# Kernel tuning notes

Measured on AMD Instinct MI355X. Metric: run time of the kernel, lower is better.

## Reference

```python
import jax, jax.numpy as jnp
import numpy as np

BS, E, A, TE, TA = 128, 32, 8, 8, 4
V, WD, HD = 30522, 300, 1024


def gru_last(x, lengths, Wih, Whh, bih, bhh):
    """Single-layer unidirectional GRU (torch gate math); returns h at step lengths-1.
    x: [N, T, D], lengths: [N] (>=1)."""
    N, T, D = x.shape
    xp = jnp.einsum('ntd,gd->ntg', x, Wih) + bih  # [N, T, 3D]
    h0 = jnp.zeros((N, D), x.dtype)

    def step(h, args):
        xpt, t = args
        gh = h @ Whh.T + bhh
        xr, xz, xn = jnp.split(xpt, 3, axis=-1)
        hr, hz, hn = jnp.split(gh, 3, axis=-1)
        r = jax.nn.sigmoid(xr + hr)
        z = jax.nn.sigmoid(xz + hz)
        n = jnp.tanh(xn + r * hn)
        h_new = (1.0 - z) * n + z * h
        h = jnp.where((t < lengths)[:, None], h_new, h)  # freeze after length
        return h, None

    hT, _ = jax.lax.scan(step, h0, (jnp.transpose(xp, (1, 0, 2)), jnp.arange(T)))
    return hT


def setup_inputs() -> dict:
    key = jax.random.key(0)
    ks = jax.random.split(key, 20)
    s = 0.05
    p = lambda k, shp: jax.random.normal(k, shp, dtype=jnp.float32) * s
    return {
        'entity_tokens': jax.random.randint(ks[0], (BS, E, TE), 0, V),
        'entity_lengths': jax.random.randint(ks[1], (BS, E), 1, TE + 1),
        'entity_padding_mask': jnp.zeros((BS, E, TE), dtype=bool),
        'entity_attribute_tokens': jax.random.randint(ks[2], (BS, E, A, TA), 0, V),
        'entity_attribute_lengths': jax.random.randint(ks[3], (BS, E, A), 1, TA + 1),
        'entity_attribute_padding_mask': jnp.zeros((BS, E, A, TA), dtype=bool),
        'emb_table': p(ks[4], (V, WD)),
        'Wih_ent': p(ks[5], (3 * WD, WD)),
        'Whh_ent': p(ks[6], (3 * WD, WD)),
        'bih_ent': jnp.zeros((3 * WD,), jnp.float32),
        'bhh_ent': jnp.zeros((3 * WD,), jnp.float32),
        'Wih_attr': p(ks[7], (3 * WD, WD)),
        'Whh_attr': p(ks[8], (3 * WD, WD)),
        'bih_attr': jnp.zeros((3 * WD,), jnp.float32),
        'bhh_attr': jnp.zeros((3 * WD,), jnp.float32),
        'Wfc': p(ks[9], (HD, WD)),
        'bfc': jnp.zeros((HD,), jnp.float32),
        'Wg': p(ks[10], (HD, HD)),
        'a_src': p(ks[11], (HD,)),
        'a_dst': p(ks[12], (HD,)),
    }


def reference(entity_tokens, entity_lengths, entity_padding_mask,
              entity_attribute_tokens, entity_attribute_lengths, entity_attribute_padding_mask,
              emb_table, Wih_ent, Whh_ent, bih_ent, bhh_ent,
              Wih_attr, Whh_attr, bih_attr, bhh_attr,
              Wfc, bfc, Wg, a_src, a_dst):
    bs, nE, tE = entity_tokens.shape
    nA, tA = entity_attribute_tokens.shape[2], entity_attribute_tokens.shape[3]
    G = bs * nE
    N = nA + 1  # 1 entity node + nA attribute nodes per small star graph

    # --- embed entity phrases (GRU over tokens, take last valid state) ---
    ent_len = jnp.clip(entity_lengths.reshape(-1), 1, None)
    ent_x = emb_table[entity_tokens.reshape(G, tE)]  # [G, tE, WD]
    ent_h = gru_last(ent_x, ent_len, Wih_ent, Whh_ent, bih_ent, bhh_ent)
    ent = jax.nn.relu(ent_h @ Wfc.T + bfc)  # [G, HD]

    # --- embed attribute phrases ---
    at_len = jnp.clip(entity_attribute_lengths.reshape(-1), 1, None)
    at_x = emb_table[entity_attribute_tokens.reshape(G * nA, tA)]
    at_h = gru_last(at_x, at_len, Wih_attr, Whh_attr, bih_attr, bhh_attr)
    attr = jax.nn.relu(at_h @ Wfc.T + bfc).reshape(G, nA, -1)  # [G, nA, HD]

    # --- adjacency: entity node 0 linked to each valid attribute; self loop on node 0 ---
    valid = ((~entity_attribute_padding_mask).sum(-1) > 0).reshape(G, nA).astype(jnp.float32)
    adj = jnp.zeros((G, N, N), jnp.float32)
    adj = adj.at[:, 1:, 0].set(valid)
    adj = adj.at[:, 0, 0].set(1.0)
    adj = adj + jnp.transpose(adj, (0, 2, 1))
    adj = adj > 1e-5  # bool mask

    # --- GAT-style masked node attention ---
    nodes = jnp.concatenate([ent[:, None, :], attr], axis=1)  # [G, N, HD]
    h = nodes @ Wg.T
    es = h @ a_src  # [G, N]
    ed = h @ a_dst
    e = jax.nn.leaky_relu(es[:, :, None] + ed[:, None, :], 0.2)
    e = jnp.where(adj, e, -1e9)
    alpha = jax.nn.softmax(e, axis=-1)
    out = jax.nn.elu(jnp.einsum('gij,gjd->gid', alpha, h))

    entity_embeds = out[:, 0, :].reshape(bs, nE, -1)  # hidden_dim == embed_dim -> no fc_out
    return entity_embeds
```

## Files before the change

### kernel.cpp

```cpp
#include <hip/hip_runtime.h>
#include <math.h>

namespace {

typedef unsigned short bf16_t;
typedef __bf16  bf16x8_t __attribute__((ext_vector_type(8)));
typedef float   f32x4_t  __attribute__((ext_vector_type(4)));
typedef unsigned int u32x4 __attribute__((ext_vector_type(4)));

constexpr int G     = 4096;
constexpr int GA    = 32768;
constexpr int WDIM  = 300;
constexpr int KPAD  = 320;
constexpr int HDIM  = 1024;
constexpr int NNODE = 9;
constexpr int MROWS = G * NNODE;
constexpr int TE_   = 8;
constexpr int TA_   = 4;
constexpr int V_    = 30522;
constexpr int VP    = 30592;
constexpr int PROJW = 1024;

__device__ __forceinline__ float bf2f(bf16_t b) {
    union { unsigned int u; float f; } v; v.u = ((unsigned int)b) << 16; return v.f;
}
__device__ __forceinline__ bf16_t f2bf(float f) {
    union { float f; unsigned int u; } v; v.f = f;
    unsigned int r = v.u + 0x7FFFu + ((v.u >> 16) & 1u);
    return (bf16_t)(r >> 16);
}

template<int MODE>
__global__ __launch_bounds__(256)
void mfma_gemm(const bf16_t* __restrict__ A, const bf16_t* __restrict__ B,
               void* __restrict__ Cv, int lda, int ldb, int ldc, int K)
{
    __shared__ bf16_t As[128 * 32];
    __shared__ bf16_t Bs[128 * 32];

    const int tid  = threadIdx.x;
    const int w    = tid >> 6;
    const int lane = tid & 63;
    const int wr = w >> 1, wc = w & 1;
    const int lr = lane & 15;
    const int lk = lane >> 4;
    const int m0 = blockIdx.x * 128, n0 = blockIdx.y * 128;

    const int r0 = tid >> 2;
    const int cc = (tid & 3) * 8;
    const bf16_t* Arow0 = A + (size_t)(m0 + r0) * lda + cc;
    const bf16_t* Arow1 = Arow0 + (size_t)64 * lda;
    const bf16_t* Brow0 = B + (size_t)(n0 + r0) * ldb + cc;
    const bf16_t* Brow1 = Brow0 + (size_t)64 * ldb;

    f32x4_t acc[4][4];
#pragma unroll
    for (int i = 0; i < 4; ++i)
#pragma unroll
        for (int j = 0; j < 4; ++j) acc[i][j] = {0.f, 0.f, 0.f, 0.f};

    for (int k0 = 0; k0 < K; k0 += 32) {
        const uint4 a0 = *(const uint4*)(Arow0 + k0);
        const uint4 a1 = *(const uint4*)(Arow1 + k0);
        const uint4 b0 = *(const uint4*)(Brow0 + k0);
        const uint4 b1 = *(const uint4*)(Brow1 + k0);
        __syncthreads();
        *(uint4*)&As[r0 * 32 + cc]        = a0;
        *(uint4*)&As[(r0 + 64) * 32 + cc] = a1;
        *(uint4*)&Bs[r0 * 32 + cc]        = b0;
        *(uint4*)&Bs[(r0 + 64) * 32 + cc] = b1;
        __syncthreads();

        bf16x8_t af[4], bfr[4];
#pragma unroll
        for (int i = 0; i < 4; ++i) {
            af[i]  = *(const bf16x8_t*)&As[(wr * 64 + i * 16 + lr) * 32 + lk * 8];
            bfr[i] = *(const bf16x8_t*)&Bs[(wc * 64 + i * 16 + lr) * 32 + lk * 8];
        }
#pragma unroll
        for (int mi = 0; mi < 4; ++mi)
#pragma unroll
            for (int ni = 0; ni < 4; ++ni)
                acc[mi][ni] = __builtin_amdgcn_mfma_f32_16x16x32_bf16(
                    af[mi], bfr[ni], acc[mi][ni], 0, 0, 0);
    }

#pragma unroll
    for (int mi = 0; mi < 4; ++mi) {
#pragma unroll
        for (int ni = 0; ni < 4; ++ni) {
            const int n = n0 + wc * 64 + ni * 16 + lr;
#pragma unroll
            for (int r = 0; r < 4; ++r) {
                const int m = m0 + wr * 64 + mi * 16 + lk * 4 + r;
                const float v = acc[mi][ni][r];
                if (MODE == 0)
                    ((bf16_t*)Cv)[(size_t)m * ldc + n] = f2bf(v);
                else
                    ((float*)Cv)[(size_t)m * ldc + n] = v > 0.f ? v : expm1f(v);
            }
        }
    }
}

__global__ __launch_bounds__(512)
void gru_step_fused(const bf16_t* __restrict__ hin,
                    bf16_t* __restrict__ hout,
                    const bf16_t* __restrict__ Whh3i,
                    const bf16_t* __restrict__ proj,
                    const int* __restrict__ tokens,
                    const int* __restrict__ lengths,
                    const float* __restrict__ bih, const float* __restrict__ bhh,
                    int T, int t)
{
    constexpr int GSTRF = 123;
    __shared__ __align__(16) bf16_t As[128 * 32];
    __shared__ __align__(16) bf16_t Bs[128 * 32];
    __shared__ float gsm[128 * GSTRF];

    const int tid = threadIdx.x;
    const int w = tid >> 6, lane = tid & 63;
    const int lr = lane & 15, lk = lane >> 4;
    const int wr = w >> 2, wc = w & 3;
    const int m0 = blockIdx.x * 128;
    const int nb = blockIdx.y;
    const int n0 = nb * 120;

    const int sr = tid >> 2, sc = (tid & 3) * 8;
    const bf16_t* Ap = hin   + (size_t)(m0 + sr) * KPAD + sc;
    const bf16_t* Bp = Whh3i + (size_t)(n0 + sr) * KPAD + sc;

    f32x4_t acc[4][2];
#pragma unroll
    for (int mi = 0; mi < 4; ++mi)
#pragma unroll
        for (int ni = 0; ni < 2; ++ni) acc[mi][ni] = {0.f, 0.f, 0.f, 0.f};

    for (int k0 = 0; k0 < KPAD; k0 += 32) {
        const uint4 av = *(const uint4*)(Ap + k0);
        const uint4 bv = *(const uint4*)(Bp + k0);
        __syncthreads();
        *(uint4*)&As[sr * 32 + sc] = av;
        *(uint4*)&Bs[sr * 32 + sc] = bv;
        __syncthreads();

        bf16x8_t af[4], bfr[2];
#pragma unroll
        for (int mi = 0; mi < 4; ++mi)
            af[mi] = *(const bf16x8_t*)&As[(wr * 64 + mi * 16 + lr) * 32 + lk * 8];
#pragma unroll
        for (int ni = 0; ni < 2; ++ni)
            bfr[ni] = *(const bf16x8_t*)&Bs[(wc * 32 + ni * 16 + lr) * 32 + lk * 8];
#pragma unroll
        for (int mi = 0; mi < 4; ++mi)
#pragma unroll
            for (int ni = 0; ni < 2; ++ni)
                acc[mi][ni] = __builtin_amdgcn_mfma_f32_16x16x32_bf16(
                    af[mi], bfr[ni], acc[mi][ni], 0, 0, 0);
    }

#pragma unroll
    for (int ni = 0; ni < 2; ++ni) {
        const int col = wc * 32 + ni * 16 + lr;
        if (col < 120) {
#pragma unroll
            for (int mi = 0; mi < 4; ++mi)
#pragma unroll
                for (int r = 0; r < 4; ++r)
                    gsm[(wr * 64 + mi * 16 + lk * 4 + r) * GSTRF + col]
                        = acc[mi][ni][r];
        }
    }
    __syncthreads();

    const int ml = tid >> 2, q = tid & 3;
    if (nb == 7 && q >= 2) return;
    const int m  = m0 + ml;
    const int jb = nb * 40 + q * 10;
    int len = lengths[m]; if (len < 1) len = 1;
    const bool act = (t < len);
    const int tok = tokens[(size_t)m * T + t];

    const unsigned int* xpp =
        (const unsigned int*)(proj + (size_t)tok * PROJW + n0 + q * 30);
    unsigned int xw[15];
#pragma unroll
    for (int i = 0; i < 15; ++i) xw[i] = xpp[i];

    const unsigned int* hop = (const unsigned int*)(hin + (size_t)m * KPAD + jb);
    unsigned int hw[5];
#pragma unroll
    for (int i = 0; i < 5; ++i) hw[i] = hop[i];

    unsigned int ow[5];
#pragma unroll
    for (int u = 0; u < 10; ++u) {
        const int j = jb + u;
        const bf16_t hob = (bf16_t)((u & 1) ? (hw[u >> 1] >> 16) : (hw[u >> 1] & 0xffff));
        const float hold = bf2f(hob);
        float hv = hold;
        if (act) {
            const int e0 = 3 * u;
            const float xr = bf2f((bf16_t)((e0 & 1)       ? (xw[e0 >> 1] >> 16)       : (xw[e0 >> 1] & 0xffff)));
            const float xz = bf2f((bf16_t)(((e0 + 1) & 1) ? (xw[(e0 + 1) >> 1] >> 16) : (xw[(e0 + 1) >> 1] & 0xffff)));
            const float xn = bf2f((bf16_t)(((e0 + 2) & 1) ? (xw[(e0 + 2) >> 1] >> 16) : (xw[(e0 + 2) >> 1] & 0xffff)));
            const int nl = q * 30 + 3 * u;
            const float g0 = gsm[ml * GSTRF + nl];
            const float g1 = gsm[ml * GSTRF + nl + 1];
            const float g2 = gsm[ml * GSTRF + nl + 2];
            const float rr = 1.f / (1.f + expf(-(g0 + xr + bih[j] + bhh[j])));
            const float zz = 1.f / (1.f + expf(-(g1 + xz + bih[WDIM + j] + bhh[WDIM + j])));
            const float nn = tanhf(xn + bih[2 * WDIM + j] + rr * (g2 + bhh[2 * WDIM + j]));
            hv = (1.f - zz) * nn + zz * hold;
        }
        const bf16_t hb_ = f2bf(hv);
        if ((u & 1) == 0) ow[u >> 1] = hb_;
        else              ow[u >> 1] |= ((unsigned int)hb_) << 16;
    }
    unsigned int* outp = (unsigned int*)(hout + (size_t)m * KPAD + jb);
#pragma unroll
    for (int i = 0; i < 5; ++i) outp[i] = ow[i];
}

__global__ __launch_bounds__(256)
void fc_nodes_esed(const bf16_t* __restrict__ hEnt, const bf16_t* __restrict__ hAtt,
                   const bf16_t* __restrict__ WfcB, const float* __restrict__ bfc,
                   const float* __restrict__ asW, const float* __restrict__ adW,
                   bf16_t* __restrict__ nodes, float* __restrict__ es, float* __restrict__ ed)
{
    constexpr int ASTR = 328;
    __shared__ bf16_t As[64 * ASTR];
    __shared__ bf16_t Bs[64 * 32];
    __shared__ const bf16_t* rowp[64];

    const int tid = threadIdx.x;
    const int w = tid >> 6, lane = tid & 63;
    const int lr = lane & 15, lk = lane >> 4;
    const int m0 = blockIdx.x * 64;

    if (tid < 64) {
        const int m = m0 + tid;
        const int g = m / NNODE, i = m - g * NNODE;
        rowp[tid] = (i == 0) ? (hEnt + (size_t)g * KPAD)
                             : (hAtt + (size_t)(g * 8 + (i - 1)) * KPAD);
    }
    __syncthreads();

#pragma unroll
    for (int it = 0; it < 10; ++it) {
        const int i = tid + 256 * it;
        const int row = i / 40, c8 = (i - row * 40) * 8;
        const uint4 v = *(const uint4*)(rowp[row] + c8);
        *(uint4*)&As[row * ASTR + c8] = v;
    }
    __syncthreads();

    float esa[4] = {0.f, 0.f, 0.f, 0.f};
    float eda[4] = {0.f, 0.f, 0.f, 0.f};

    for (int nt = 0; nt < 16; ++nt) {
        const int n0 = nt * 64;
        f32x4_t acc[4];
#pragma unroll
        for (int ni = 0; ni < 4; ++ni) acc[ni] = {0.f, 0.f, 0.f, 0.f};

        for (int k0 = 0; k0 < KPAD; k0 += 32) {
            const int rr_ = tid >> 2, c8 = (tid & 3) * 8;
            const uint4 bv = *(const uint4*)(WfcB + (size_t)(n0 + rr_) * KPAD + k0 + c8);
            __syncthreads();
            *(uint4*)&Bs[rr_ * 32 + c8] = bv;
            __syncthreads();

            const bf16x8_t af = *(const bf16x8_t*)&As[(w * 16 + lr) * ASTR + k0 + lk * 8];
#pragma unroll
            for (int ni = 0; ni < 4; ++ni) {
                const bf16x8_t bfr = *(const bf16x8_t*)&Bs[(ni * 16 + lr) * 32 + lk * 8];
                acc[ni] = __builtin_amdgcn_mfma_f32_16x16x32_bf16(af, bfr, acc[ni], 0, 0, 0);
            }
        }

#pragma unroll
        for (int ni = 0; ni < 4; ++ni) {
            const int n = n0 + ni * 16 + lr;
            const float aw = asW[n], dw = adW[n], bb = bfc[n];
#pragma unroll
            for (int r = 0; r < 4; ++r) {
                float v = acc[ni][r] + bb;
                v = v > 0.f ? v : 0.f;
                const int m = m0 + w * 16 + lk * 4 + r;
                nodes[(size_t)m * HDIM + n] = f2bf(v);
                esa[r] = fmaf(v, aw, esa[r]);
                eda[r] = fmaf(v, dw, eda[r]);
            }
        }
    }

#pragma unroll
    for (int r = 0; r < 4; ++r) {
        float s = esa[r], d = eda[r];
#pragma unroll
        for (int mask = 1; mask < 16; mask <<= 1) {
            s += __shfl_xor(s, mask, 64);
            d += __shfl_xor(d, mask, 64);
        }
        if (lr == 0) {
            const int m = m0 + w * 16 + lk * 4 + r;
            es[m] = s; ed[m] = d;
        }
    }
}

__global__ __launch_bounds__(256)
void convert_emb_kernel(const float* __restrict__ emb, bf16_t* __restrict__ embB)
{
    const int idx = blockIdx.x * 256 + threadIdx.x;
    if (idx >= V_ * 40) return;
    const int row = idx / 40, c8 = (idx - row * 40) * 8;
    bf16_t o[8];
#pragma unroll
    for (int e = 0; e < 8; ++e) {
        const int c = c8 + e;
        o[e] = (c < WDIM) ? f2bf(emb[(size_t)row * WDIM + c]) : (bf16_t)0;
    }
    *(ushort4*)(embB + (size_t)row * KPAD + c8)     = *(ushort4*)&o[0];
    *(ushort4*)(embB + (size_t)row * KPAD + c8 + 4) = *(ushort4*)&o[4];
}

__global__ __launch_bounds__(256)
void build_w3i_kernel(const float* __restrict__ W, bf16_t* __restrict__ dst)
{
    const int idx = blockIdx.x * 256 + threadIdx.x;
    if (idx >= HDIM * KPAD) return;
    const int n = idx / KPAD, k = idx - n * KPAD;
    float v = 0.f;
    if (n < 960) {
        const int j = n / 3, g = n - j * 3;
        if (j < WDIM && k < WDIM)
            v = W[(size_t)(g * WDIM + j) * WDIM + k];
    }
    dst[idx] = f2bf(v);
}

__global__ __launch_bounds__(256)
void build_wfc_kernel(const float* __restrict__ Wfc, bf16_t* __restrict__ Wb)
{
    const int idx = blockIdx.x * 256 + threadIdx.x;
    if (idx >= HDIM * KPAD) return;
    const int n = idx / KPAD, k = idx - n * KPAD;
    Wb[idx] = f2bf(k < WDIM ? Wfc[(size_t)n * WDIM + k] : 0.f);
}

__global__ __launch_bounds__(256)
void build_wg_kernel(const float* __restrict__ Wg, bf16_t* __restrict__ Wb)
{
    const int idx = blockIdx.x * 256 + threadIdx.x;
    Wb[idx] = f2bf(Wg[idx]);
}

__global__ __launch_bounds__(256)
void asw_kernel(const float* __restrict__ Wg,
                const float* __restrict__ a_src, const float* __restrict__ a_dst,
                float* __restrict__ asW, float* __restrict__ adW)
{
    const int k = blockIdx.x * 256 + threadIdx.x;
    float s = 0.f, d = 0.f;
    for (int n = 0; n < HDIM; ++n) {
        const float w = Wg[(size_t)n * HDIM + k];
        s = fmaf(a_src[n], w, s);
        d = fmaf(a_dst[n], w, d);
    }
    asW[k] = s; adW[k] = d;
}

__global__ __launch_bounds__(256)
void attn_mix_kernel(const bf16_t* __restrict__ nodes,
                     const float* __restrict__ es, const float* __restrict__ ed,
                     bf16_t* __restrict__ mixed)
{
    const int g = blockIdx.x;
    const float e0 = es[(size_t)g * NNODE];
    const float* edg = ed + (size_t)g * NNODE;

    float w[NNODE], mx = -1e30f;
#pragma unroll
    for (int j = 0; j < NNODE; ++j) {
        float v = e0 + edg[j];
        v = v >= 0.f ? v : 0.2f * v;
        w[j] = v; mx = fmaxf(mx, v);
    }
    float denom = 0.f;
#pragma unroll
    for (int j = 0; j < NNODE; ++j) { w[j] = expf(w[j] - mx); denom += w[j]; }
    const float inv = 1.f / denom;

    const int c = threadIdx.x * 4;
    float4 acc = {0.f, 0.f, 0.f, 0.f};
#pragma unroll
    for (int j = 0; j < NNODE; ++j) {
        const float a = w[j] * inv;
        const ushort4 h4 = *(const ushort4*)(nodes + (size_t)(g * NNODE + j) * HDIM + c);
        acc.x = fmaf(a, bf2f(h4.x), acc.x);
        acc.y = fmaf(a, bf2f(h4.y), acc.y);
        acc.z = fmaf(a, bf2f(h4.z), acc.z);
        acc.w = fmaf(a, bf2f(h4.w), acc.w);
    }
    ushort4 o;
    o.x = f2bf(acc.x); o.y = f2bf(acc.y); o.z = f2bf(acc.z); o.w = f2bf(acc.w);
    *(ushort4*)(mixed + (size_t)g * HDIM + c) = o;
}

constexpr size_t SZ_EMBB  = (size_t)VP * KPAD * sizeof(bf16_t);
constexpr size_t SZ_PROJ  = (size_t)VP * PROJW * sizeof(bf16_t);
constexpr size_t SZ_HATT  = (size_t)GA * KPAD * sizeof(bf16_t);
constexpr size_t SZ_HENT  = (size_t)G * KPAD * sizeof(bf16_t);
constexpr size_t SZ_WIH3  = (size_t)HDIM * KPAD * sizeof(bf16_t);
constexpr size_t SZ_WHH3E = (size_t)HDIM * KPAD * sizeof(bf16_t);
constexpr size_t SZ_WFC   = (size_t)HDIM * KPAD * sizeof(bf16_t);
constexpr size_t SZ_WG    = (size_t)HDIM * HDIM * sizeof(bf16_t);
constexpr size_t SZ_AW    = (size_t)HDIM * sizeof(float);
constexpr size_t SZ_VEC   = (size_t)MROWS * sizeof(float);
constexpr size_t SZ_NODE  = (size_t)MROWS * HDIM * sizeof(bf16_t);
constexpr size_t SZ_MIX   = (size_t)G * HDIM * sizeof(bf16_t);
constexpr size_t WS_NEED  = SZ_EMBB + SZ_PROJ + 2 * SZ_HATT + 2 * SZ_HENT +
                            SZ_WIH3 + 2 * SZ_WHH3E + SZ_WFC + SZ_WG +
                            2 * SZ_AW + 2 * SZ_VEC;
static_assert(SZ_NODE <= SZ_EMBB + SZ_PROJ, "nodes overlays embB+proj");
static_assert(SZ_MIX  <= 2 * SZ_HATT,       "mixed overlays hAtt pair");

}

extern "C" void kernel_launch(void* const* d_in, const int* in_sizes, int n_in,
                              void* d_out, int out_size, void* d_ws, size_t ws_size,
                              hipStream_t stream)
{
    (void)in_sizes; (void)n_in; (void)out_size;
    if (ws_size < WS_NEED) return;

    const int*   ent_tok  = (const int*)  d_in[0];
    const int*   ent_len  = (const int*)  d_in[1];
    const int*   at_tok   = (const int*)  d_in[3];
    const int*   at_len   = (const int*)  d_in[4];
    const float* emb      = (const float*)d_in[6];
    const float* Wih_ent  = (const float*)d_in[7];
    const float* Whh_ent  = (const float*)d_in[8];
    const float* bih_ent  = (const float*)d_in[9];
    const float* bhh_ent  = (const float*)d_in[10];
    const float* Wih_attr = (const float*)d_in[11];
    const float* Whh_attr = (const float*)d_in[12];
    const float* bih_attr = (const float*)d_in[13];
    const float* bhh_attr = (const float*)d_in[14];
    const float* Wfc      = (const float*)d_in[15];
    const float* bfc      = (const float*)d_in[16];
    const float* Wg       = (const float*)d_in[17];
    const float* a_src    = (const float*)d_in[18];
    const float* a_dst    = (const float*)d_in[19];
    float* out = (float*)d_out;

    char* p = (char*)d_ws;
    bf16_t* embB  = (bf16_t*)p; p += SZ_EMBB;
    bf16_t* proj  = (bf16_t*)p; p += SZ_PROJ;
    bf16_t* hAtt[2];
    hAtt[0] = (bf16_t*)p; p += SZ_HATT;
    hAtt[1] = (bf16_t*)p; p += SZ_HATT;
    bf16_t* hEnt   = (bf16_t*)p; p += SZ_HENT;
    bf16_t* hEnt2  = (bf16_t*)p; p += SZ_HENT;
    bf16_t* Wih3   = (bf16_t*)p; p += SZ_WIH3;
    bf16_t* Whh3_a = (bf16_t*)p; p += SZ_WHH3E;
    bf16_t* Whh3_e = (bf16_t*)p; p += SZ_WHH3E;
    bf16_t* WfcB   = (bf16_t*)p; p += SZ_WFC;
    bf16_t* WgB    = (bf16_t*)p; p += SZ_WG;
    float*  asW    = (float*)p;  p += SZ_AW;
    float*  adW    = (float*)p;  p += SZ_AW;
    float*  es     = (float*)p;  p += SZ_VEC;
    float*  ed     = (float*)p;  p += SZ_VEC;
    bf16_t* nodes  = embB;
    bf16_t* mixed  = hAtt[0];

    hipMemsetAsync(hAtt[0], 0, SZ_HATT, stream);
    hipMemsetAsync(hAtt[1], 0, SZ_HATT, stream);
    hipMemsetAsync(hEnt,  0, SZ_HENT, stream);
    hipMemsetAsync(hEnt2, 0, SZ_HENT, stream);

    convert_emb_kernel<<<dim3((V_ * 40 + 255) / 256), 256, 0, stream>>>(emb, embB);
    build_w3i_kernel<<<dim3(HDIM * KPAD / 256), 256, 0, stream>>>(Wih_attr, Wih3);
    build_w3i_kernel<<<dim3(HDIM * KPAD / 256), 256, 0, stream>>>(Whh_attr, Whh3_a);
    build_w3i_kernel<<<dim3(HDIM * KPAD / 256), 256, 0, stream>>>(Whh_ent, Whh3_e);
    build_wfc_kernel<<<dim3(HDIM * KPAD / 256), 256, 0, stream>>>(Wfc, WfcB);
    build_wg_kernel<<<dim3(HDIM * HDIM / 256), 256, 0, stream>>>(Wg, WgB);
    asw_kernel<<<dim3(HDIM / 256), 256, 0, stream>>>(Wg, a_src, a_dst, asW, adW);

    mfma_gemm<0><<<dim3(VP / 128, PROJW / 128), 256, 0, stream>>>(
        embB, Wih3, proj, KPAD, KPAD, PROJW, KPAD);

    for (int t = 0; t < TA_; ++t)
        gru_step_fused<<<dim3(GA / 128, 8), 512, 0, stream>>>(
            hAtt[t & 1], hAtt[(t + 1) & 1], Whh3_a, proj, at_tok, at_len,
            bih_attr, bhh_attr, TA_, t);

    build_w3i_kernel<<<dim3(HDIM * KPAD / 256), 256, 0, stream>>>(Wih_ent, Wih3);
    mfma_gemm<0><<<dim3(VP / 128, PROJW / 128), 256, 0, stream>>>(
        embB, Wih3, proj, KPAD, KPAD, PROJW, KPAD);

    bf16_t* hb[2] = { hEnt, hEnt2 };
    for (int t = 0; t < TE_; ++t)
        gru_step_fused<<<dim3(G / 128, 8), 512, 0, stream>>>(
            hb[t & 1], hb[(t + 1) & 1], Whh3_e, proj, ent_tok, ent_len,
            bih_ent, bhh_ent, TE_, t);

    fc_nodes_esed<<<dim3(MROWS / 64), 256, 0, stream>>>(
        hEnt, hAtt[0], WfcB, bfc, asW, adW, nodes, es, ed);

    attn_mix_kernel<<<dim3(G), 256, 0, stream>>>(nodes, es, ed, mixed);

    mfma_gemm<2><<<dim3(G / 128, HDIM / 128), 256, 0, stream>>>(
        mixed, WgB, out, HDIM, HDIM, HDIM, HDIM);
}
```

Baseline: 779.6 us.

## Pad GEMM LDS rows and split fc_nodes into tiled GEMM plus es/ed kernel

The shared-memory tiles in the generic MFMA GEMM get a row stride of 40 instead of 32, which is meant to reduce LDS bank conflicts on fragment reads. The fused fc_nodes_esed kernel, which gave each block 64 rows and looped over all 1024 output columns, is replaced by a 2D-tiled 128x128 GEMM. Its es/ed attention-score dot products move into a separate kernel that re-reads the bf16 nodes. This adds parallelism and reuse to the FC GEMM, at the cost of an extra launch and an extra pass over the nodes buffer. es/ed are now computed from bf16-rounded values rather than fp32, a small numerical change.

```diff
diff --git a/kernel.cpp b/kernel.cpp
--- a/kernel.cpp
+++ b/kernel.cpp
@@ -35,8 +35,9 @@
 void mfma_gemm(const bf16_t* __restrict__ A, const bf16_t* __restrict__ B,
                void* __restrict__ Cv, int lda, int ldb, int ldc, int K)
 {
-    __shared__ bf16_t As[128 * 32];
-    __shared__ bf16_t Bs[128 * 32];
+    constexpr int AST = 40;
+    __shared__ __align__(16) bf16_t As[128 * AST];
+    __shared__ __align__(16) bf16_t Bs[128 * AST];
 
     const int tid  = threadIdx.x;
     const int w    = tid >> 6;
@@ -65,17 +66,17 @@
         const uint4 b0 = *(const uint4*)(Brow0 + k0);
         const uint4 b1 = *(const uint4*)(Brow1 + k0);
         __syncthreads();
-        *(uint4*)&As[r0 * 32 + cc]        = a0;
-        *(uint4*)&As[(r0 + 64) * 32 + cc] = a1;
-        *(uint4*)&Bs[r0 * 32 + cc]        = b0;
-        *(uint4*)&Bs[(r0 + 64) * 32 + cc] = b1;
+        *(uint4*)&As[r0 * AST + cc]        = a0;
+        *(uint4*)&As[(r0 + 64) * AST + cc] = a1;
+        *(uint4*)&Bs[r0 * AST + cc]        = b0;
+        *(uint4*)&Bs[(r0 + 64) * AST + cc] = b1;
         __syncthreads();
 
         bf16x8_t af[4], bfr[4];
 #pragma unroll
         for (int i = 0; i < 4; ++i) {
-            af[i]  = *(const bf16x8_t*)&As[(wr * 64 + i * 16 + lr) * 32 + lk * 8];
-            bfr[i] = *(const bf16x8_t*)&Bs[(wc * 64 + i * 16 + lr) * 32 + lk * 8];
+            af[i]  = *(const bf16x8_t*)&As[(wr * 64 + i * 16 + lr) * AST + lk * 8];
+            bfr[i] = *(const bf16x8_t*)&Bs[(wc * 64 + i * 16 + lr) * AST + lk * 8];
         }
 #pragma unroll
         for (int mi = 0; mi < 4; ++mi)
@@ -223,22 +224,24 @@
 }
 
 __global__ __launch_bounds__(256)
-void fc_nodes_esed(const bf16_t* __restrict__ hEnt, const bf16_t* __restrict__ hAtt,
+void fc_nodes_gemm(const bf16_t* __restrict__ hEnt, const bf16_t* __restrict__ hAtt,
                    const bf16_t* __restrict__ WfcB, const float* __restrict__ bfc,
-                   const float* __restrict__ asW, const float* __restrict__ adW,
-                   bf16_t* __restrict__ nodes, float* __restrict__ es, float* __restrict__ ed)
-{
-    constexpr int ASTR = 328;
-    __shared__ bf16_t As[64 * ASTR];
-    __shared__ bf16_t Bs[64 * 32];
-    __shared__ const bf16_t* rowp[64];
-
-    const int tid = threadIdx.x;
-    const int w = tid >> 6, lane = tid & 63;
-    const int lr = lane & 15, lk = lane >> 4;
-    const int m0 = blockIdx.x * 64;
-
-    if (tid < 64) {
+                   bf16_t* __restrict__ nodes)
+{
+    constexpr int AST = 40;
+    __shared__ __align__(16) bf16_t As[128 * AST];
+    __shared__ __align__(16) bf16_t Bs[128 * AST];
+    __shared__ const bf16_t* rowp[128];
+
+    const int tid  = threadIdx.x;
+    const int w    = tid >> 6;
+    const int lane = tid & 63;
+    const int wr = w >> 1, wc = w & 1;
+    const int lr = lane & 15;
+    const int lk = lane >> 4;
+    const int m0 = blockIdx.x * 128, n0 = blockIdx.y * 128;
+
+    if (tid < 128) {
         const int m = m0 + tid;
         const int g = m / NNODE, i = m - g * NNODE;
         rowp[tid] = (i == 0) ? (hEnt + (size_t)g * KPAD)
@@ -246,68 +249,96 @@
     }
     __syncthreads();
 
-#pragma unroll
-    for (int it = 0; it < 10; ++it) {
-        const int i = tid + 256 * it;
-        const int row = i / 40, c8 = (i - row * 40) * 8;
-        const uint4 v = *(const uint4*)(rowp[row] + c8);
-        *(uint4*)&As[row * ASTR + c8] = v;
-    }
-    __syncthreads();
-
-    float esa[4] = {0.f, 0.f, 0.f, 0.f};
-    float eda[4] = {0.f, 0.f, 0.f, 0.f};
-
-    for (int nt = 0; nt < 16; ++nt) {
-        const int n0 = nt * 64;
-        f32x4_t acc[4];
-#pragma unroll
-        for (int ni = 0; ni < 4; ++ni) acc[ni] = {0.f, 0.f, 0.f, 0.f};
-
-        for (int k0 = 0; k0 < KPAD; k0 += 32) {
-            const int rr_ = tid >> 2, c8 = (tid & 3) * 8;
-            const uint4 bv = *(const uint4*)(WfcB + (size_t)(n0 + rr_) * KPAD + k0 + c8);
-            __syncthreads();
-            *(uint4*)&Bs[rr_ * 32 + c8] = bv;
-            __syncthreads();
-
-            const bf16x8_t af = *(const bf16x8_t*)&As[(w * 16 + lr) * ASTR + k0 + lk * 8];
-#pragma unroll
-            for (int ni = 0; ni < 4; ++ni) {
-                const bf16x8_t bfr = *(const bf16x8_t*)&Bs[(ni * 16 + lr) * 32 + lk * 8];
-                acc[ni] = __builtin_amdgcn_mfma_f32_16x16x32_bf16(af, bfr, acc[ni], 0, 0, 0);
+    const int r0 = tid >> 2;
+    const int cc = (tid & 3) * 8;
+    const bf16_t* Arow0 = rowp[r0] + cc;
+    const bf16_t* Arow1 = rowp[r0 + 64] + cc;
+    const bf16_t* Brow0 = WfcB + (size_t)(n0 + r0) * KPAD + cc;
+    const bf16_t* Brow1 = Brow0 + (size_t)64 * KPAD;
+
+    f32x4_t acc[4][4];
+#pragma unroll
+    for (int i = 0; i < 4; ++i)
+#pragma unroll
+        for (int j = 0; j < 4; ++j) acc[i][j] = {0.f, 0.f, 0.f, 0.f};
+
+    for (int k0 = 0; k0 < KPAD; k0 += 32) {
+        const uint4 a0 = *(const uint4*)(Arow0 + k0);
+        const uint4 a1 = *(const uint4*)(Arow1 + k0);
+        const uint4 b0 = *(const uint4*)(Brow0 + k0);
+        const uint4 b1 = *(const uint4*)(Brow1 + k0);
+        __syncthreads();
+        *(uint4*)&As[r0 * AST + cc]        = a0;
+        *(uint4*)&As[(r0 + 64) * AST + cc] = a1;
+        *(uint4*)&Bs[r0 * AST + cc]        = b0;
+        *(uint4*)&Bs[(r0 + 64) * AST + cc] = b1;
+        __syncthreads();
+
+        bf16x8_t af[4], bfr[4];
+#pragma unroll
+        for (int i = 0; i < 4; ++i) {
+            af[i]  = *(const bf16x8_t*)&As[(wr * 64 + i * 16 + lr) * AST + lk * 8];
+            bfr[i] = *(const bf16x8_t*)&Bs[(wc * 64 + i * 16 + lr) * AST + lk * 8];
+        }
+#pragma unroll
+        for (int mi = 0; mi < 4; ++mi)
+#pragma unroll
+            for (int ni = 0; ni < 4; ++ni)
+                acc[mi][ni] = __builtin_amdgcn_mfma_f32_16x16x32_bf16(
+                    af[mi], bfr[ni], acc[mi][ni], 0, 0, 0);
+    }
+
+#pragma unroll
+    for (int mi = 0; mi < 4; ++mi) {
+#pragma unroll
+        for (int ni = 0; ni < 4; ++ni) {
+            const int n = n0 + wc * 64 + ni * 16 + lr;
+            const float bb = bfc[n];
+#pragma unroll
+            for (int r = 0; r < 4; ++r) {
+                const int m = m0 + wr * 64 + mi * 16 + lk * 4 + r;
+                float v = acc[mi][ni][r] + bb;
+                v = v > 0.f ? v : 0.f;
+                nodes[(size_t)m * HDIM + n] = f2bf(v);
             }
         }
-
-#pragma unroll
-        for (int ni = 0; ni < 4; ++ni) {
-            const int n = n0 + ni * 16 + lr;
-            const float aw = asW[n], dw = adW[n], bb = bfc[n];
-#pragma unroll
-            for (int r = 0; r < 4; ++r) {
-                float v = acc[ni][r] + bb;
-                v = v > 0.f ? v : 0.f;
-                const int m = m0 + w * 16 + lk * 4 + r;
-                nodes[(size_t)m * HDIM + n] = f2bf(v);
-                esa[r] = fmaf(v, aw, esa[r]);
-                eda[r] = fmaf(v, dw, eda[r]);
-            }
-        }
-    }
-
-#pragma unroll
-    for (int r = 0; r < 4; ++r) {
-        float s = esa[r], d = eda[r];
-#pragma unroll
-        for (int mask = 1; mask < 16; mask <<= 1) {
-            s += __shfl_xor(s, mask, 64);
-            d += __shfl_xor(d, mask, 64);
-        }
-        if (lr == 0) {
-            const int m = m0 + w * 16 + lk * 4 + r;
-            es[m] = s; ed[m] = d;
-        }
-    }
+    }
+}
+
+__global__ __launch_bounds__(256)
+void esed_kernel(const bf16_t* __restrict__ nodes,
+                 const float* __restrict__ asW, const float* __restrict__ adW,
+                 float* __restrict__ es, float* __restrict__ ed)
+{
+    const int m    = (blockIdx.x * 256 + threadIdx.x) >> 6;
+    const int lane = threadIdx.x & 63;
+    const bf16_t* row = nodes + (size_t)m * HDIM;
+
+    const uint4 v0 = *(const uint4*)(row + lane * 8);
+    const uint4 v1 = *(const uint4*)(row + 512 + lane * 8);
+
+    float s = 0.f, d = 0.f;
+    const unsigned int* w0 = (const unsigned int*)&v0;
+    const unsigned int* w1 = (const unsigned int*)&v1;
+#pragma unroll
+    for (int e = 0; e < 4; ++e) {
+        const int c0 = lane * 8 + 2 * e;
+        const float x0 = bf2f((bf16_t)(w0[e] & 0xffff));
+        const float x1 = bf2f((bf16_t)(w0[e] >> 16));
+        s = fmaf(x0, asW[c0], s);     s = fmaf(x1, asW[c0 + 1], s);
+        d = fmaf(x0, adW[c0], d);     d = fmaf(x1, adW[c0 + 1], d);
+        const int c1 = 512 + lane * 8 + 2 * e;
+        const float y0 = bf2f((bf16_t)(w1[e] & 0xffff));
+        const float y1 = bf2f((bf16_t)(w1[e] >> 16));
+        s = fmaf(y0, asW[c1], s);     s = fmaf(y1, asW[c1 + 1], s);
+        d = fmaf(y0, adW[c1], d);     d = fmaf(y1, adW[c1 + 1], d);
+    }
+#pragma unroll
+    for (int mask = 1; mask < 64; mask <<= 1) {
+        s += __shfl_xor(s, mask, 64);
+        d += __shfl_xor(d, mask, 64);
+    }
+    if (lane == 0) { es[m] = s; ed[m] = d; }
 }
 
 __global__ __launch_bounds__(256)
@@ -507,8 +538,10 @@
             hb[t & 1], hb[(t + 1) & 1], Whh3_e, proj, ent_tok, ent_len,
             bih_ent, bhh_ent, TE_, t);
 
-    fc_nodes_esed<<<dim3(MROWS / 64), 256, 0, stream>>>(
-        hEnt, hAtt[0], WfcB, bfc, asW, adW, nodes, es, ed);
+    fc_nodes_gemm<<<dim3(MROWS / 128, HDIM / 128), 256, 0, stream>>>(
+        hEnt, hAtt[0], WfcB, bfc, nodes);
+
+    esed_kernel<<<dim3(MROWS / 4), 256, 0, stream>>>(nodes, asW, adW, es, ed);
 
     attn_mix_kernel<<<dim3(G), 256, 0, stream>>>(nodes, es, ed, mixed);
 
```

New measurement: 767.7 us. No clear change (-1.5%).
